# Performance work log

Measured on AMD Instinct MI355X. Metric: run time of the kernel, lower is better.

Reference implementation:

```python
import jax, jax.numpy as jnp
import numpy as np

B, T, C = 2, 8192, 1024
H, BS, LW = 16, 64, 128          # num_heads, block_size, local_window_size
D = C // H                        # head_dim = 64
W = BS + LW                       # max window length per block = 192
NB = T // BS                      # number of blocks


def setup_inputs() -> dict:
    key = jax.random.key(0)
    ks = jax.random.split(key, 11)
    s = 1.0 / np.sqrt(C)          # small init so softmax is not saturated
    return {
        'query': jax.random.normal(ks[0], (B, T, C), jnp.float32),
        'key':   jax.random.normal(ks[1], (B, T, C), jnp.float32),
        'value': jax.random.normal(ks[2], (B, T, C), jnp.float32),
        'Wq': jax.random.normal(ks[3], (C, C), jnp.float32) * s,
        'bq': jax.random.normal(ks[4], (C,), jnp.float32) * s,
        'Wk': jax.random.normal(ks[5], (C, C), jnp.float32) * s,
        'bk': jax.random.normal(ks[6], (C,), jnp.float32) * s,
        'Wv': jax.random.normal(ks[7], (C, C), jnp.float32) * s,
        'bv': jax.random.normal(ks[8], (C,), jnp.float32) * s,
        'Wo': jax.random.normal(ks[9], (C, C), jnp.float32) * s,
        'bo': jax.random.normal(ks[10], (C,), jnp.float32) * s,
    }


def reference(query, key, value, Wq, bq, Wk, bk, Wv, bv, Wo, bo):
    # projections -> (B, H, T, D)
    def proj(x, Wt, bt):
        return (x @ Wt.T + bt).reshape(B, T, H, D).transpose(0, 2, 1, 3)

    scale = jnp.asarray(D, query.dtype) ** -0.5
    q = proj(query, Wq, bq) * scale
    k = proj(key, Wk, bk)
    v = proj(value, Wv, bv)

    # per-block window indices: block i attends to [i - LW//2, i + BS + LW//2)
    starts = jnp.arange(NB) * BS                              # (NB,)
    idx = starts[:, None] + jnp.arange(-LW // 2, BS + LW // 2)  # (NB, W)
    valid = (idx >= 0) & (idx < T)                            # (NB, W)
    cidx = jnp.clip(idx, 0, T - 1)

    q_blk = q.reshape(B, H, NB, BS, D)
    k_win = k[:, :, cidx, :]                                  # (B, H, NB, W, D)
    v_win = v[:, :, cidx, :]

    scores = jnp.einsum('bhnqd,bhnkd->bhnqk', q_blk, k_win).astype(jnp.float32)
    scores = jnp.where(valid[None, None, :, None, :], scores, -jnp.inf)
    probs = jax.nn.softmax(scores, axis=-1).astype(q.dtype)

    out = jnp.einsum('bhnqk,bhnkd->bhnqd', probs, v_win)      # (B, H, NB, BS, D)
    out = out.reshape(B, H, T, D).transpose(0, 2, 1, 3).reshape(B, T, C)
    return out @ Wo.T + bo
```

## Files before the change

### kernel.cpp

```cpp
#include <hip/hip_runtime.h>
#include <hip/hip_bf16.h>
#include <type_traits>

#define BATCH 2
#define SEQ   8192
#define CH    1024
#define NH    16
#define BLK   64
#define WIN   192
#define NBL   128
#define DH    64
#define MR    (BATCH*SEQ)

typedef __bf16 bf16x8 __attribute__((ext_vector_type(8)));
typedef float  f32x4  __attribute__((ext_vector_type(4)));

__device__ __forceinline__ f32x4 zero4() {
    f32x4 z; z[0]=0.f; z[1]=0.f; z[2]=0.f; z[3]=0.f; return z;
}

union Pack8 { __hip_bfloat16 h[8]; uint4 u; };

typedef const __attribute__((address_space(1))) unsigned int* gas_ptr;
typedef       __attribute__((address_space(3))) unsigned int* las_ptr;

__device__ __forceinline__ void gload_lds16(const __hip_bfloat16* g, __hip_bfloat16* l) {
    __builtin_amdgcn_global_load_lds((gas_ptr)(const void*)g, (las_ptr)(void*)l, 16, 0, 0);
}

__global__ __launch_bounds__(256) void pack_bf16(
    const float* __restrict__ src, __hip_bfloat16* __restrict__ dst, int n8)
{
    int i = blockIdx.x * 256 + threadIdx.x;
    if (i >= n8) return;
    const float4* s = reinterpret_cast<const float4*>(src);
    float4 a = s[2 * i], b = s[2 * i + 1];
    Pack8 p;
    p.h[0] = __float2bfloat16(a.x); p.h[1] = __float2bfloat16(a.y);
    p.h[2] = __float2bfloat16(a.z); p.h[3] = __float2bfloat16(a.w);
    p.h[4] = __float2bfloat16(b.x); p.h[5] = __float2bfloat16(b.y);
    p.h[6] = __float2bfloat16(b.z); p.h[7] = __float2bfloat16(b.w);
    reinterpret_cast<uint4*>(dst)[i] = p.u;
}

template<typename OT>
__device__ __forceinline__ void gemm_body(
    const __hip_bfloat16* __restrict__ A, const __hip_bfloat16* __restrict__ Wb,
    const float* __restrict__ bias, OT* __restrict__ out, float alpha,
    __hip_bfloat16* As, __hip_bfloat16* Bs)
{
    const int tid  = threadIdx.x;
    const int m0   = blockIdx.y * 128;
    const int n0   = blockIdx.x * 128;
    const int wid  = tid >> 6;
    const int lane = tid & 63;
    const int quad = lane >> 4;
    const int l16  = lane & 15;
    const int wr   = wid >> 1, wc = wid & 1;

    int offA[4], offB[4];
    #pragma unroll
    for (int it = 0; it < 4; it++) {
        int c = tid + it * 256;
        int r = c >> 3;
        int s = (c & 7) ^ (r & 7);
        offA[it] = (m0 + r) * CH + s * 8;
        offB[it] = (n0 + r) * CH + s * 8;
    }

    f32x4 acc[4][4];
    #pragma unroll
    for (int i = 0; i < 4; i++)
        #pragma unroll
        for (int j = 0; j < 4; j++) acc[i][j] = zero4();

    for (int k0 = 0; k0 < CH; k0 += 64) {
        #pragma unroll
        for (int it = 0; it < 4; it++)
            gload_lds16(A + offA[it] + k0, As + (tid + it * 256) * 8);
        #pragma unroll
        for (int it = 0; it < 4; it++)
            gload_lds16(Wb + offB[it] + k0, Bs + (tid + it * 256) * 8);
        __syncthreads();

        #pragma unroll
        for (int kk = 0; kk < 2; kk++) {
            bf16x8 af[4], bfr[4];
            #pragma unroll
            for (int i = 0; i < 4; i++) {
                int r = wr * 64 + i * 16 + l16;
                int chunk = r * 8 + ((kk * 4 + quad) ^ (l16 & 7));
                af[i] = *reinterpret_cast<const bf16x8*>(As + chunk * 8);
            }
            #pragma unroll
            for (int j = 0; j < 4; j++) {
                int r = wc * 64 + j * 16 + l16;
                int chunk = r * 8 + ((kk * 4 + quad) ^ (l16 & 7));
                bfr[j] = *reinterpret_cast<const bf16x8*>(Bs + chunk * 8);
            }
            #pragma unroll
            for (int i = 0; i < 4; i++)
                #pragma unroll
                for (int j = 0; j < 4; j++)
                    acc[i][j] = __builtin_amdgcn_mfma_f32_16x16x32_bf16(
                        af[i], bfr[j], acc[i][j], 0, 0, 0);
        }
        __syncthreads();
    }

    #pragma unroll
    for (int j = 0; j < 4; j++) {
        const int col = n0 + wc * 64 + j * 16 + l16;
        const float bv = bias[col];
        #pragma unroll
        for (int i = 0; i < 4; i++) {
            #pragma unroll
            for (int r = 0; r < 4; r++) {
                const int row = m0 + wr * 64 + i * 16 + quad * 4 + r;
                float v = alpha * (acc[i][j][r] + bv);
                if constexpr (std::is_same<OT, float>::value)
                    out[(size_t)row * CH + col] = v;
                else
                    out[(size_t)row * CH + col] = __float2bfloat16(v);
            }
        }
    }
}

__global__ __launch_bounds__(256) void gemm_qk(
    const __hip_bfloat16* __restrict__ A0, const __hip_bfloat16* __restrict__ W0,
    const float* __restrict__ b0, __hip_bfloat16* __restrict__ o0, float alpha0,
    const __hip_bfloat16* __restrict__ A1, const __hip_bfloat16* __restrict__ W1,
    const float* __restrict__ b1, __hip_bfloat16* __restrict__ o1)
{
    __shared__ alignas(16) __hip_bfloat16 As[128 * 64];
    __shared__ alignas(16) __hip_bfloat16 Bs[128 * 64];
    if (blockIdx.z == 0)
        gemm_body<__hip_bfloat16>(A0, W0, b0, o0, alpha0, As, Bs);
    else
        gemm_body<__hip_bfloat16>(A1, W1, b1, o1, 1.0f, As, Bs);
}

template<typename OT>
__global__ __launch_bounds__(256) void gemm_one(
    const __hip_bfloat16* __restrict__ A, const __hip_bfloat16* __restrict__ Wb,
    const float* __restrict__ bias, OT* __restrict__ out)
{
    __shared__ alignas(16) __hip_bfloat16 As[128 * 64];
    __shared__ alignas(16) __hip_bfloat16 Bs[128 * 64];
    gemm_body<OT>(A, Wb, bias, out, 1.0f, As, Bs);
}

__global__ __launch_bounds__(256) void attn_kernel(
    const __hip_bfloat16* __restrict__ qg,
    const __hip_bfloat16* __restrict__ kg,
    const __hip_bfloat16* __restrict__ vg,
    __hip_bfloat16* __restrict__ ctx)
{
    __shared__ alignas(16) char smem[62464];
    auto qs = reinterpret_cast<__hip_bfloat16(*)[72]>(smem);
    auto ks = reinterpret_cast<__hip_bfloat16(*)[72]>(smem + 9216);
    auto vt = reinterpret_cast<__hip_bfloat16(*)[200]>(smem + 36864);
    auto ps = reinterpret_cast<__hip_bfloat16(*)[200]>(smem);

    const int blk = blockIdx.x;
    const int n = blk & (NBL - 1);
    const int h = (blk >> 7) & (NH - 1);
    const int b = blk >> 11;
    const int t0  = n * BLK;
    const int kst = t0 - 64;
    const int tid = threadIdx.x;
    const size_t baseBH = (size_t)b * SEQ * CH + (size_t)h * DH;

    #pragma unroll
    for (int it = 0; it < 2; it++) {
        int c = tid + it * 256;
        int row = c >> 3, seg = c & 7;
        *reinterpret_cast<uint4*>(&qs[row][seg * 8]) =
            *reinterpret_cast<const uint4*>(qg + baseBH + (size_t)(t0 + row) * CH + seg * 8);
    }
    #pragma unroll
    for (int it = 0; it < 6; it++) {
        int c = tid + it * 256;
        int row = c >> 3, seg = c & 7;
        int tr = kst + row; tr = tr < 0 ? 0 : (tr >= SEQ ? SEQ - 1 : tr);
        *reinterpret_cast<uint4*>(&ks[row][seg * 8]) =
            *reinterpret_cast<const uint4*>(kg + baseBH + (size_t)tr * CH + seg * 8);
    }
    #pragma unroll
    for (int it = 0; it < 6; it++) {
        int c = tid + it * 256;
        int j = c % WIN, seg = c / WIN;
        int tr = kst + j; tr = tr < 0 ? 0 : (tr >= SEQ ? SEQ - 1 : tr);
        Pack8 p;
        p.u = *reinterpret_cast<const uint4*>(vg + baseBH + (size_t)tr * CH + seg * 8);
        #pragma unroll
        for (int e = 0; e < 8; e++) vt[seg * 8 + e][j] = p.h[e];
    }
    __syncthreads();

    const int wid = tid >> 6, lane = tid & 63, quad = lane >> 4, l16 = lane & 15;

    f32x4 sc[12];
    #pragma unroll
    for (int j = 0; j < 12; j++) sc[j] = zero4();
    #pragma unroll
    for (int kk = 0; kk < 2; kk++) {
        bf16x8 aq = *reinterpret_cast<const bf16x8*>(&qs[wid * 16 + l16][kk * 32 + quad * 8]);
        #pragma unroll
        for (int j = 0; j < 12; j++) {
            bf16x8 bk = *reinterpret_cast<const bf16x8*>(&ks[j * 16 + l16][kk * 32 + quad * 8]);
            sc[j] = __builtin_amdgcn_mfma_f32_16x16x32_bf16(aq, bk, sc[j], 0, 0, 0);
        }
    }
    __syncthreads();

    #pragma unroll
    for (int r = 0; r < 4; r++) {
        float s[12];
        float mx = -3.0e38f;
        #pragma unroll
        for (int j = 0; j < 12; j++) {
            int col = j * 16 + l16;
            int tr = kst + col;
            bool valid = (tr >= 0) && (tr < SEQ);
            s[j] = valid ? sc[j][r] : -3.0e38f;
            mx = fmaxf(mx, s[j]);
        }
        #pragma unroll
        for (int o = 1; o < 16; o <<= 1) mx = fmaxf(mx, __shfl_xor(mx, o, 64));
        float sum = 0.f;
        #pragma unroll
        for (int j = 0; j < 12; j++) {
            float e = __expf(s[j] - mx);
            s[j] = e;
            sum += e;
        }
        #pragma unroll
        for (int o = 1; o < 16; o <<= 1) sum += __shfl_xor(sum, o, 64);
        const float inv = 1.f / sum;
        const int row = wid * 16 + quad * 4 + r;
        #pragma unroll
        for (int j = 0; j < 12; j++)
            ps[row][j * 16 + l16] = __float2bfloat16(s[j] * inv);
    }
    __syncthreads();

    f32x4 oa[4];
    #pragma unroll
    for (int j = 0; j < 4; j++) oa[j] = zero4();
    #pragma unroll
    for (int kk = 0; kk < 6; kk++) {
        bf16x8 ap = *reinterpret_cast<const bf16x8*>(&ps[wid * 16 + l16][kk * 32 + quad * 8]);
        #pragma unroll
        for (int j = 0; j < 4; j++) {
            bf16x8 bv = *reinterpret_cast<const bf16x8*>(&vt[j * 16 + l16][kk * 32 + quad * 8]);
            oa[j] = __builtin_amdgcn_mfma_f32_16x16x32_bf16(ap, bv, oa[j], 0, 0, 0);
        }
    }
    #pragma unroll
    for (int j = 0; j < 4; j++) {
        const int d = j * 16 + l16;
        #pragma unroll
        for (int r = 0; r < 4; r++) {
            const int i = wid * 16 + quad * 4 + r;
            ctx[baseBH + (size_t)(t0 + i) * CH + d] = __float2bfloat16(oa[j][r]);
        }
    }
}

extern "C" void kernel_launch(void* const* d_in, const int* in_sizes, int n_in,
                              void* d_out, int out_size, void* d_ws, size_t ws_size,
                              hipStream_t stream)
{
    const float* query = (const float*)d_in[0];
    const float* key_i = (const float*)d_in[1];
    const float* value = (const float*)d_in[2];
    const float* Wq = (const float*)d_in[3];
    const float* bq = (const float*)d_in[4];
    const float* Wk = (const float*)d_in[5];
    const float* bk = (const float*)d_in[6];
    const float* Wv = (const float*)d_in[7];
    const float* bv = (const float*)d_in[8];
    const float* Wo = (const float*)d_in[9];
    const float* bo = (const float*)d_in[10];
    float* out = (float*)d_out;

    const size_t NELEM = (size_t)MR * CH;
    const size_t WELEM = (size_t)CH * CH;

    __hip_bfloat16* S0 = (__hip_bfloat16*)d_ws;
    __hip_bfloat16* S1 = S0 + NELEM;
    __hip_bfloat16* S2 = S1 + NELEM;
    __hip_bfloat16* S3 = S2 + NELEM;
    __hip_bfloat16* wqb = S3;
    __hip_bfloat16* wkb = S3 + WELEM;
    __hip_bfloat16* wvb = S3 + 2 * WELEM;
    __hip_bfloat16* wob = S3 + 3 * WELEM;

    __hip_bfloat16* xq = (__hip_bfloat16*)d_out;
    __hip_bfloat16* xk = xq + NELEM;
    __hip_bfloat16* vb = (__hip_bfloat16*)d_out;
    __hip_bfloat16* qb = S1;
    __hip_bfloat16* kb = S2;
    __hip_bfloat16* cb = S0;

    const int nA8 = (int)(NELEM / 8);
    const int nW8 = (int)(WELEM / 8);

    pack_bf16<<<nA8 / 256, 256, 0, stream>>>(query, xq, nA8);
    pack_bf16<<<nA8 / 256, 256, 0, stream>>>(key_i, xk, nA8);
    pack_bf16<<<nA8 / 256, 256, 0, stream>>>(value, S0, nA8);
    pack_bf16<<<nW8 / 256, 256, 0, stream>>>(Wq, wqb, nW8);
    pack_bf16<<<nW8 / 256, 256, 0, stream>>>(Wk, wkb, nW8);
    pack_bf16<<<nW8 / 256, 256, 0, stream>>>(Wv, wvb, nW8);
    pack_bf16<<<nW8 / 256, 256, 0, stream>>>(Wo, wob, nW8);

    dim3 ggrid(CH / 128, MR / 128);
    dim3 qkgrid(CH / 128, MR / 128, 2);

    gemm_qk<<<qkgrid, 256, 0, stream>>>(xq, wqb, bq, qb, 0.125f,
                                        xk, wkb, bk, kb);
    gemm_one<__hip_bfloat16><<<ggrid, 256, 0, stream>>>(S0, wvb, bv, vb);

    attn_kernel<<<BATCH * NH * NBL, 256, 0, stream>>>(qb, kb, vb, cb);

    gemm_one<float><<<ggrid, 256, 0, stream>>>(cb, wob, bo, out);
}
```

Measured before the change: 502.0 us.

## Use 256x256 double-buffered GEMM tiles with phased prefetch and XCD swizzle

Replaces the 128x128 single-buffered projection GEMM with a 256x256-tile, 512-thread kernel. It double-buffers LDS and interleaves async global-to-LDS loads of the next K slab with MFMA phases, using manual waitcnt, barriers and setprio. Workgroup IDs are remapped across XCDs for the GEMMs and the attention kernel to improve L2 locality. The cost is 128KB of LDS per block, which limits occupancy, plus fragile hand-written synchronization counts.

```diff
diff --git a/kernel.cpp b/kernel.cpp
--- a/kernel.cpp
+++ b/kernel.cpp
@@ -26,6 +26,10 @@
 
 __device__ __forceinline__ void gload_lds16(const __hip_bfloat16* g, __hip_bfloat16* l) {
     __builtin_amdgcn_global_load_lds((gas_ptr)(const void*)g, (las_ptr)(void*)l, 16, 0, 0);
+}
+
+__device__ __forceinline__ int xcd_swz(int bid, int nwg) {
+    return (bid & 7) * (nwg >> 3) + (bid >> 3);
 }
 
 __global__ __launch_bounds__(256) void pack_bf16(
@@ -43,80 +47,134 @@
     reinterpret_cast<uint4*>(dst)[i] = p.u;
 }
 
+
+__device__ __forceinline__ void stage_half(
+    const __hip_bfloat16* __restrict__ g, int goff,
+    __hip_bfloat16* sm, int loff, int tid)
+{
+    gload_lds16(g + goff,            sm + loff + tid * 8);
+    gload_lds16(g + goff + 128 * CH, sm + loff + (tid + 512) * 8);
+}
+
+template<int MH, int KS>
+__device__ __forceinline__ void phase_mfma(
+    const __hip_bfloat16* As_, const __hip_bfloat16* Bs_,
+    int aoff, int boff, f32x4 (&acc)[8][4])
+{
+    bf16x8 af[4], bf[4];
+    #pragma unroll
+    for (int i = 0; i < 4; ++i)
+        af[i] = *reinterpret_cast<const bf16x8*>(As_ + KS * 8192 + (MH * 4 + i) * 512 + aoff);
+    #pragma unroll
+    for (int j = 0; j < 4; ++j)
+        bf[j] = *reinterpret_cast<const bf16x8*>(Bs_ + KS * 8192 + j * 512 + boff);
+    asm volatile("s_waitcnt lgkmcnt(0)" ::: "memory");
+    __builtin_amdgcn_sched_barrier(0);
+    __builtin_amdgcn_s_setprio(1);
+    #pragma unroll
+    for (int i = 0; i < 4; ++i)
+        #pragma unroll
+        for (int j = 0; j < 4; ++j)
+            acc[MH * 4 + i][j] = __builtin_amdgcn_mfma_f32_16x16x32_bf16(
+                af[i], bf[j], acc[MH * 4 + i][j], 0, 0, 0);
+    __builtin_amdgcn_s_setprio(0);
+}
+
 template<typename OT>
-__device__ __forceinline__ void gemm_body(
+__device__ __forceinline__ void gemm_body256(
     const __hip_bfloat16* __restrict__ A, const __hip_bfloat16* __restrict__ Wb,
     const float* __restrict__ bias, OT* __restrict__ out, float alpha,
-    __hip_bfloat16* As, __hip_bfloat16* Bs)
+    int m0, int n0, __hip_bfloat16* sm)
 {
     const int tid  = threadIdx.x;
-    const int m0   = blockIdx.y * 128;
-    const int n0   = blockIdx.x * 128;
     const int wid  = tid >> 6;
     const int lane = tid & 63;
     const int quad = lane >> 4;
     const int l16  = lane & 15;
-    const int wr   = wid >> 1, wc = wid & 1;
-
-    int offA[4], offB[4];
-    #pragma unroll
-    for (int it = 0; it < 4; it++) {
-        int c = tid + it * 256;
-        int r = c >> 3;
-        int s = (c & 7) ^ (r & 7);
-        offA[it] = (m0 + r) * CH + s * 8;
-        offB[it] = (n0 + r) * CH + s * 8;
-    }
-
-    f32x4 acc[4][4];
-    #pragma unroll
-    for (int i = 0; i < 4; i++)
-        #pragma unroll
-        for (int j = 0; j < 4; j++) acc[i][j] = zero4();
-
-    for (int k0 = 0; k0 < CH; k0 += 64) {
-        #pragma unroll
-        for (int it = 0; it < 4; it++)
-            gload_lds16(A + offA[it] + k0, As + (tid + it * 256) * 8);
-        #pragma unroll
-        for (int it = 0; it < 4; it++)
-            gload_lds16(Wb + offB[it] + k0, Bs + (tid + it * 256) * 8);
-        __syncthreads();
-
-        #pragma unroll
-        for (int kk = 0; kk < 2; kk++) {
-            bf16x8 af[4], bfr[4];
-            #pragma unroll
-            for (int i = 0; i < 4; i++) {
-                int r = wr * 64 + i * 16 + l16;
-                int chunk = r * 8 + ((kk * 4 + quad) ^ (l16 & 7));
-                af[i] = *reinterpret_cast<const bf16x8*>(As + chunk * 8);
-            }
-            #pragma unroll
-            for (int j = 0; j < 4; j++) {
-                int r = wc * 64 + j * 16 + l16;
-                int chunk = r * 8 + ((kk * 4 + quad) ^ (l16 & 7));
-                bfr[j] = *reinterpret_cast<const bf16x8*>(Bs + chunk * 8);
-            }
-            #pragma unroll
-            for (int i = 0; i < 4; i++)
-                #pragma unroll
-                for (int j = 0; j < 4; j++)
-                    acc[i][j] = __builtin_amdgcn_mfma_f32_16x16x32_bf16(
-                        af[i], bfr[j], acc[i][j], 0, 0, 0);
-        }
-        __syncthreads();
-    }
-
-    #pragma unroll
-    for (int j = 0; j < 4; j++) {
+    const int wr   = wid >> 2, wc = wid & 3;
+
+    const int r0 = tid >> 2;
+    const int s0 = (tid & 3) ^ (r0 & 3);
+    const int offA0 = (m0 + r0) * CH + s0 * 8;
+    const int offB0 = (n0 + r0) * CH + s0 * 8;
+
+    const int cq   = quad ^ (l16 & 3);
+    const int aoff = ((wr * 128 + l16) * 4 + cq) * 8;
+    const int boff = ((wc * 64  + l16) * 4 + cq) * 8;
+
+    f32x4 acc[8][4];
+    #pragma unroll
+    for (int i = 0; i < 8; ++i)
+        #pragma unroll
+        for (int j = 0; j < 4; ++j) acc[i][j] = zero4();
+
+    stage_half(A,  offA0,      sm, 0,             tid);
+    stage_half(Wb, offB0,      sm, 32768,         tid);
+    stage_half(A,  offA0 + 32, sm, 8192,          tid);
+    stage_half(Wb, offB0 + 32, sm, 32768 + 8192,  tid);
+
+    #pragma unroll 1
+    for (int t = 0; t < 15; ++t) {
+        const int cur = t & 1, nb = cur ^ 1;
+        const int kn  = (t + 1) * 64;
+        const __hip_bfloat16* As_ = sm + cur * 16384;
+        const __hip_bfloat16* Bs_ = sm + 32768 + cur * 16384;
+
+        asm volatile("s_waitcnt vmcnt(4)" ::: "memory");
+        __builtin_amdgcn_s_barrier();
+        __builtin_amdgcn_sched_barrier(0);
+        stage_half(A, offA0 + kn, sm, nb * 16384, tid);
+        phase_mfma<0, 0>(As_, Bs_, aoff, boff, acc);
+
+        __builtin_amdgcn_s_barrier();
+        __builtin_amdgcn_sched_barrier(0);
+        stage_half(Wb, offB0 + kn, sm, 32768 + nb * 16384, tid);
+        phase_mfma<1, 0>(As_, Bs_, aoff, boff, acc);
+
+        asm volatile("s_waitcnt vmcnt(4)" ::: "memory");
+        __builtin_amdgcn_s_barrier();
+        __builtin_amdgcn_sched_barrier(0);
+        stage_half(A, offA0 + kn + 32, sm, nb * 16384 + 8192, tid);
+        phase_mfma<0, 1>(As_, Bs_, aoff, boff, acc);
+
+        __builtin_amdgcn_s_barrier();
+        __builtin_amdgcn_sched_barrier(0);
+        stage_half(Wb, offB0 + kn + 32, sm, 32768 + nb * 16384 + 8192, tid);
+        phase_mfma<1, 1>(As_, Bs_, aoff, boff, acc);
+    }
+
+    {
+        const __hip_bfloat16* As_ = sm + 16384;
+        const __hip_bfloat16* Bs_ = sm + 32768 + 16384;
+
+        asm volatile("s_waitcnt vmcnt(4)" ::: "memory");
+        __builtin_amdgcn_s_barrier();
+        __builtin_amdgcn_sched_barrier(0);
+        phase_mfma<0, 0>(As_, Bs_, aoff, boff, acc);
+
+        __builtin_amdgcn_s_barrier();
+        __builtin_amdgcn_sched_barrier(0);
+        phase_mfma<1, 0>(As_, Bs_, aoff, boff, acc);
+
+        asm volatile("s_waitcnt vmcnt(0)" ::: "memory");
+        __builtin_amdgcn_s_barrier();
+        __builtin_amdgcn_sched_barrier(0);
+        phase_mfma<0, 1>(As_, Bs_, aoff, boff, acc);
+
+        __builtin_amdgcn_s_barrier();
+        __builtin_amdgcn_sched_barrier(0);
+        phase_mfma<1, 1>(As_, Bs_, aoff, boff, acc);
+    }
+
+    #pragma unroll
+    for (int j = 0; j < 4; ++j) {
         const int col = n0 + wc * 64 + j * 16 + l16;
         const float bv = bias[col];
         #pragma unroll
-        for (int i = 0; i < 4; i++) {
+        for (int i = 0; i < 8; ++i) {
             #pragma unroll
-            for (int r = 0; r < 4; r++) {
-                const int row = m0 + wr * 64 + i * 16 + quad * 4 + r;
+            for (int r = 0; r < 4; ++r) {
+                const int row = m0 + wr * 128 + i * 16 + quad * 4 + r;
                 float v = alpha * (acc[i][j][r] + bv);
                 if constexpr (std::is_same<OT, float>::value)
                     out[(size_t)row * CH + col] = v;
@@ -127,28 +185,35 @@
     }
 }
 
-__global__ __launch_bounds__(256) void gemm_qk(
+__device__ __forceinline__ void gemm_tile256(int& m0, int& n0) {
+    int bid = blockIdx.y * 4 + blockIdx.x;
+    int swz = (bid & 7) * 32 + (bid >> 3);
+    m0 = (swz >> 2) * 256;
+    n0 = (swz & 3) * 256;
+}
+
+__global__ __launch_bounds__(512, 2) void gemm_qk256(
     const __hip_bfloat16* __restrict__ A0, const __hip_bfloat16* __restrict__ W0,
     const float* __restrict__ b0, __hip_bfloat16* __restrict__ o0, float alpha0,
     const __hip_bfloat16* __restrict__ A1, const __hip_bfloat16* __restrict__ W1,
     const float* __restrict__ b1, __hip_bfloat16* __restrict__ o1)
 {
-    __shared__ alignas(16) __hip_bfloat16 As[128 * 64];
-    __shared__ alignas(16) __hip_bfloat16 Bs[128 * 64];
+    __shared__ alignas(16) __hip_bfloat16 sm[65536];
+    int m0, n0; gemm_tile256(m0, n0);
     if (blockIdx.z == 0)
-        gemm_body<__hip_bfloat16>(A0, W0, b0, o0, alpha0, As, Bs);
+        gemm_body256<__hip_bfloat16>(A0, W0, b0, o0, alpha0, m0, n0, sm);
     else
-        gemm_body<__hip_bfloat16>(A1, W1, b1, o1, 1.0f, As, Bs);
+        gemm_body256<__hip_bfloat16>(A1, W1, b1, o1, 1.0f, m0, n0, sm);
 }
 
 template<typename OT>
-__global__ __launch_bounds__(256) void gemm_one(
+__global__ __launch_bounds__(512, 2) void gemm_one256(
     const __hip_bfloat16* __restrict__ A, const __hip_bfloat16* __restrict__ Wb,
     const float* __restrict__ bias, OT* __restrict__ out)
 {
-    __shared__ alignas(16) __hip_bfloat16 As[128 * 64];
-    __shared__ alignas(16) __hip_bfloat16 Bs[128 * 64];
-    gemm_body<OT>(A, Wb, bias, out, 1.0f, As, Bs);
+    __shared__ alignas(16) __hip_bfloat16 sm[65536];
+    int m0, n0; gemm_tile256(m0, n0);
+    gemm_body256<OT>(A, Wb, bias, out, 1.0f, m0, n0, sm);
 }
 
 __global__ __launch_bounds__(256) void attn_kernel(
@@ -163,7 +228,7 @@
     auto vt = reinterpret_cast<__hip_bfloat16(*)[200]>(smem + 36864);
     auto ps = reinterpret_cast<__hip_bfloat16(*)[200]>(smem);
 
-    const int blk = blockIdx.x;
+    const int blk = xcd_swz(blockIdx.x, BATCH * NH * NBL);
     const int n = blk & (NBL - 1);
     const int h = (blk >> 7) & (NH - 1);
     const int b = blk >> 11;
@@ -316,14 +381,14 @@
     pack_bf16<<<nW8 / 256, 256, 0, stream>>>(Wv, wvb, nW8);
     pack_bf16<<<nW8 / 256, 256, 0, stream>>>(Wo, wob, nW8);
 
-    dim3 ggrid(CH / 128, MR / 128);
-    dim3 qkgrid(CH / 128, MR / 128, 2);
-
-    gemm_qk<<<qkgrid, 256, 0, stream>>>(xq, wqb, bq, qb, 0.125f,
-                                        xk, wkb, bk, kb);
-    gemm_one<__hip_bfloat16><<<ggrid, 256, 0, stream>>>(S0, wvb, bv, vb);
+    dim3 ggrid(CH / 256, MR / 256);
+    dim3 qkgrid(CH / 256, MR / 256, 2);
+
+    gemm_qk256<<<qkgrid, 512, 0, stream>>>(xq, wqb, bq, qb, 0.125f,
+                                           xk, wkb, bk, kb);
+    gemm_one256<__hip_bfloat16><<<ggrid, 512, 0, stream>>>(S0, wvb, bv, vb);
 
     attn_kernel<<<BATCH * NH * NBL, 256, 0, stream>>>(qb, kb, vb, cb);
 
-    gemm_one<float><<<ggrid, 256, 0, stream>>>(cb, wob, bo, out);
-}
+    gemm_one256<float><<<ggrid, 512, 0, stream>>>(cb, wob, bo, out);
+}
```

After: 451.8 us. 10.0% less time.
